# Kernel tuning notes

Measured on AMD Instinct MI355X. Metric: run time of the kernel, lower is better.

The kernel has to match this reference:

```python
import jax, jax.numpy as jnp
import numpy as np

N_NODES = 50000
N_EDGES = 800000
VOCAB = 4096          # node_emb_size
EMB_DIM = 128         # node_emb_dim
HIDDEN = 128          # hidden_dim -> layer1 out = 2*HIDDEN
N_POS = 1024


def gcn_conv(h, edge_index, W, b, n):
    """PyG GCNConv: lin -> add self loops -> sym-normalized scatter-add -> +bias."""
    h = h @ W                                   # [N, out]
    row, col = edge_index[0], edge_index[1]     # source, target
    loop = jnp.arange(n)
    row = jnp.concatenate([row, loop])
    col = jnp.concatenate([col, loop])
    deg = jax.ops.segment_sum(jnp.ones(row.shape[0], dtype=h.dtype), col, num_segments=n)
    dinv = jnp.where(deg > 0, jax.lax.rsqrt(deg), 0.0)
    norm = dinv[row] * dinv[col]                # [E+N]
    msg = h[row] * norm[:, None]                # gather + scale
    return jax.ops.segment_sum(msg, col, num_segments=n) + b


def setup_inputs() -> dict:
    key = jax.random.key(0)
    ks = jax.random.split(key, 10)
    x = jax.random.randint(ks[0], (N_NODES, 1), 0, VOCAB)
    edge_index = jax.random.randint(ks[1], (2, N_EDGES), 0, N_NODES)
    x_position = jax.random.randint(ks[2], (N_POS,), 0, N_NODES)
    # Embedding init: normal(0, emb_dim^-0.5) per initialize_parameters
    emb = jax.random.normal(ks[3], (VOCAB, EMB_DIM), jnp.float32) * EMB_DIM ** -0.5
    # GCN / linear weights (glorot-ish)
    W1 = jax.random.normal(ks[4], (EMB_DIM, 2 * HIDDEN), jnp.float32) * (EMB_DIM ** -0.5)
    b1 = jnp.zeros((2 * HIDDEN,), jnp.float32)
    W2 = jax.random.normal(ks[5], (2 * HIDDEN, HIDDEN), jnp.float32) * ((2 * HIDDEN) ** -0.5)
    b2 = jnp.zeros((HIDDEN,), jnp.float32)
    Wc = jax.random.normal(ks[6], (HIDDEN, VOCAB), jnp.float32) * (HIDDEN ** -0.5)
    bc = jnp.zeros((VOCAB,), jnp.float32)
    return {"x": x, "edge_index": edge_index, "x_position": x_position,
            "emb": emb, "W1": W1, "b1": b1, "W2": W2, "b2": b2, "Wc": Wc, "bc": bc}


def reference(x, edge_index, x_position, emb, W1, b1, W2, b2, Wc, bc):
    n = x.shape[0]
    h = emb[x[:, 0]]                                   # Embedding + squeeze(1)
    h = jax.nn.relu(gcn_conv(h, edge_index, W1, b1, n))
    z = gcn_conv(h, edge_index, W2, b2, n)             # [N, HIDDEN]
    logits = z @ Wc + bc                               # classifier over all nodes
    # embedding stage: mean of classified rows at x_position, keep dim 0
    return jnp.mean(logits[x_position], axis=0, keepdims=True)  # [1, VOCAB]
```

## Files before the change

### kernel.cpp

```cpp
#include <hip/hip_runtime.h>

constexpr int EMB  = 128;
constexpr int H1D  = 256;
constexpr int H2D  = 128;
constexpr int VOC  = 4096;
constexpr int NSL  = 32;
constexpr int RPB  = 16;

__global__ void k_pre(const float* __restrict__ emb, const float* __restrict__ W1,
                      float* __restrict__ embW1,
                      const int* __restrict__ xpos, int* count, unsigned int* flagbits,
                      int* cnt, unsigned int* needw, float* wagg, float* wsum,
                      int* nflag, int* total, int np, int n, int nwords) {
    int t = threadIdx.x;
    int b = blockIdx.x;
    if (b < VOC / RPB) {
        __shared__ float er[RPB][EMB];
        int r0 = b * RPB;
        for (int i = t; i < RPB * EMB; i += 256) {
            er[i / EMB][i % EMB] = emb[(size_t)r0 * EMB + i];
        }
        __syncthreads();
        float acc[RPB];
#pragma unroll
        for (int rr = 0; rr < RPB; rr++) acc[rr] = 0.0f;
        for (int k = 0; k < EMB; k++) {
            float w = W1[k * H1D + t];
#pragma unroll
            for (int rr = 0; rr < RPB; rr++) acc[rr] += er[rr][k] * w;
        }
#pragma unroll
        for (int rr = 0; rr < RPB; rr++) {
            embW1[(size_t)(r0 + rr) * H1D + t] = acc[rr];
        }
        return;
    }
    if (b == VOC / RPB) {
        for (int i = t; i < n; i += 256) count[i] = 0;
        for (int i = t; i < nwords; i += 256) flagbits[i] = 0u;
        __syncthreads();
        for (int p = t; p < np; p += 256) {
            int v = xpos[p];
            atomicAdd(&count[v], 1);
            atomicOr(&flagbits[v >> 5], 1u << (v & 31));
        }
        return;
    }
    int i = (b - (VOC / RPB + 1)) * 256 + t;
    if (i < n) { cnt[i] = 0; wagg[i] = 0.0f; }
    if (i < nwords) needw[i] = 0u;
    if (i < NSL * H1D) wsum[i] = 0.0f;
    if (i == 0) { *nflag = 0; *total = 0; }
}

__global__ void k_hist(const int* __restrict__ row, const int* __restrict__ col,
                       const unsigned int* __restrict__ flagbits, int* cnt,
                       unsigned int* markw, int ne) {
    int e = blockIdx.x * blockDim.x + threadIdx.x;
    int base = e * 4;
    if (base + 3 < ne) {
        int4 c4 = ((const int4*)col)[e];
        atomicAdd(&cnt[c4.x], 1);
        atomicAdd(&cnt[c4.y], 1);
        atomicAdd(&cnt[c4.z], 1);
        atomicAdd(&cnt[c4.w], 1);
        bool f0 = (flagbits[c4.x >> 5] >> (c4.x & 31)) & 1u;
        bool f1 = (flagbits[c4.y >> 5] >> (c4.y & 31)) & 1u;
        bool f2 = (flagbits[c4.z >> 5] >> (c4.z & 31)) & 1u;
        bool f3 = (flagbits[c4.w >> 5] >> (c4.w & 31)) & 1u;
        if (f0 | f1 | f2 | f3) {
            int4 r4 = ((const int4*)row)[e];
            if (f0) atomicOr(&markw[r4.x >> 5], 1u << (r4.x & 31));
            if (f1) atomicOr(&markw[r4.y >> 5], 1u << (r4.y & 31));
            if (f2) atomicOr(&markw[r4.z >> 5], 1u << (r4.z & 31));
            if (f3) atomicOr(&markw[r4.w >> 5], 1u << (r4.w & 31));
        }
    } else {
        for (int q = base; q < ne; q++) {
            int c = col[q];
            atomicAdd(&cnt[c], 1);
            if ((flagbits[c >> 5] >> (c & 31)) & 1u) {
                int r = row[q];
                atomicOr(&markw[r >> 5], 1u << (r & 31));
            }
        }
    }
}

__global__ void k_alloc(unsigned int* needw,
                        const unsigned int* __restrict__ flagbits,
                        const int* __restrict__ cnt, const int* __restrict__ count,
                        const int* __restrict__ x, int2* __restrict__ pk,
                        float* wagg, int* needlist, int* nflag, int* total,
                        int* offs, int* cursor, int n) {
    int v = blockIdx.x * blockDim.x + threadIdx.x;
    int lane = threadIdx.x & 63;
    int cv = 0;
    bool need = false;
    if (v < n) {
        cv = cnt[v];
        float dv = rsqrtf((float)cv + 1.0f);
        int2 p; p.x = x[v]; p.y = __float_as_int(dv);
        pk[v] = p;
        bool mark = (needw[v >> 5] >> (v & 31)) & 1u;
        bool flag = (flagbits[v >> 5] >> (v & 31)) & 1u;
        need = mark || flag;
        if (flag) wagg[v] = (float)count[v] / ((float)cv + 1.0f);
    }
    unsigned long long nm = __ballot(need);
    int wbase = (v & ~63) >> 5;
    if (lane == 0)  needw[wbase]     = (unsigned int)(nm & 0xffffffffu);
    if (lane == 32) needw[wbase + 1] = (unsigned int)(nm >> 32);
    int seg = need ? cv : 0;
    int incl = seg;
#pragma unroll
    for (int d = 1; d < 64; d <<= 1) {
        int t = __shfl_up(incl, d);
        if (lane >= d) incl += t;
    }
    int excl = incl - seg;
    int wave_total = __shfl(incl, 63);
    int rank = __popcll(nm & ((1ull << lane) - 1));
    int wcnt = __popcll(nm);
    int base_id = 0, base_off = 0;
    if (lane == 0) {
        if (wcnt > 0) base_id = atomicAdd(nflag, wcnt);
        if (wave_total > 0) base_off = atomicAdd(total, wave_total);
    }
    base_id  = __shfl(base_id, 0);
    base_off = __shfl(base_off, 0);
    if (need) {
        needlist[base_id + rank] = v;
        int o = base_off + excl;
        offs[v] = o;
        cursor[v] = o;
    }
}

__global__ void k_scatter(const int* __restrict__ row, const int* __restrict__ col,
                          const unsigned int* __restrict__ needw,
                          const unsigned int* __restrict__ flagbits,
                          const int* __restrict__ count,
                          const int2* __restrict__ pk,
                          int* cursor, int2* srowp, float* wagg, int ne) {
    int e = blockIdx.x * blockDim.x + threadIdx.x;
    int base = e * 4;
    auto doedge = [&](int c, int r) {
        if ((needw[c >> 5] >> (c & 31)) & 1u) {
            int pos = atomicAdd(&cursor[c], 1);
            int2 pr = pk[r];
            srowp[pos] = pr;
            if ((flagbits[c >> 5] >> (c & 31)) & 1u) {
                float dc = __int_as_float(pk[c].y);
                atomicAdd(&wagg[r], (float)count[c] * dc * __int_as_float(pr.y));
            }
        }
    };
    if (base + 3 < ne) {
        int4 c4 = ((const int4*)col)[e];
        int4 r4 = ((const int4*)row)[e];
        doedge(c4.x, r4.x);
        doedge(c4.y, r4.y);
        doedge(c4.z, r4.z);
        doedge(c4.w, r4.w);
    } else {
        for (int q = base; q < ne; q++) doedge(col[q], row[q]);
    }
}

__global__ void k_fconv(const int* __restrict__ needlist, const int* __restrict__ nneed_p,
                        const float* __restrict__ wagg, const int2* __restrict__ pk,
                        const int2* __restrict__ srowp,
                        const int* __restrict__ offs, const int* __restrict__ cnt,
                        const float* __restrict__ embW1, const float* __restrict__ b1,
                        float* __restrict__ wsum) {
    int lane = threadIdx.x & 63;
    int wib  = threadIdx.x >> 6;
    int wid  = blockIdx.x * (blockDim.x >> 6) + wib;
    int nw   = gridDim.x * (blockDim.x >> 6);
    int nn   = *nneed_p;
    const float4* __restrict__ ew = (const float4*)embW1;
    float4 bfrag = ((const float4*)b1)[lane];
    float4 acc2 = {0.0f, 0.0f, 0.0f, 0.0f};

    for (int i = wid; i < nn; i += nw) {
        int v = needlist[i];
        int2 pv = pk[v];
        float dv = __int_as_float(pv.y);
        float wa = wagg[v];
        float4 s = ew[(size_t)pv.x * 64 + lane];
        float w0 = dv * dv;
        float4 acc;
        acc.x = bfrag.x + w0 * s.x;
        acc.y = bfrag.y + w0 * s.y;
        acc.z = bfrag.z + w0 * s.z;
        acc.w = bfrag.w + w0 * s.w;
        int start = offs[v], m = cnt[v];
        for (int base = 0; base < m; base += 64) {
            int mm = min(64, m - base);
            int xr = 0; float wr = 0.0f;
            if (lane < mm) {
                int2 pke = srowp[start + base + lane];
                xr = pke.x;
                wr = __int_as_float(pke.y) * dv;
            }
            int e = 0;
            for (; e + 4 <= mm; e += 4) {
                int i0 = __shfl(xr, e),     i1 = __shfl(xr, e + 1);
                int i2 = __shfl(xr, e + 2), i3 = __shfl(xr, e + 3);
                float q0 = __shfl(wr, e),     q1 = __shfl(wr, e + 1);
                float q2 = __shfl(wr, e + 2), q3 = __shfl(wr, e + 3);
                float4 t0 = ew[(size_t)i0 * 64 + lane];
                float4 t1 = ew[(size_t)i1 * 64 + lane];
                float4 t2 = ew[(size_t)i2 * 64 + lane];
                float4 t3 = ew[(size_t)i3 * 64 + lane];
                acc.x += q0 * t0.x + q1 * t1.x + q2 * t2.x + q3 * t3.x;
                acc.y += q0 * t0.y + q1 * t1.y + q2 * t2.y + q3 * t3.y;
                acc.z += q0 * t0.z + q1 * t1.z + q2 * t2.z + q3 * t3.z;
                acc.w += q0 * t0.w + q1 * t1.w + q2 * t2.w + q3 * t3.w;
            }
            for (; e < mm; e++) {
                int i0 = __shfl(xr, e);
                float q0 = __shfl(wr, e);
                float4 t0 = ew[(size_t)i0 * 64 + lane];
                acc.x += q0 * t0.x;
                acc.y += q0 * t0.y;
                acc.z += q0 * t0.z;
                acc.w += q0 * t0.w;
            }
        }
        acc2.x += wa * fmaxf(acc.x, 0.0f);
        acc2.y += wa * fmaxf(acc.y, 0.0f);
        acc2.z += wa * fmaxf(acc.z, 0.0f);
        acc2.w += wa * fmaxf(acc.w, 0.0f);
    }

    __shared__ float red[4][H1D];
    red[wib][4 * lane + 0] = acc2.x;
    red[wib][4 * lane + 1] = acc2.y;
    red[wib][4 * lane + 2] = acc2.z;
    red[wib][4 * lane + 3] = acc2.w;
    __syncthreads();
    int t = threadIdx.x;
    float ssum = red[0][t] + red[1][t] + red[2][t] + red[3][t];
    atomicAdd(&wsum[(blockIdx.x & (NSL - 1)) * H1D + t], ssum);
}

__global__ void k_zout(const float* __restrict__ wsum, const float* __restrict__ W2,
                       const float* __restrict__ b2, const float* __restrict__ Wc,
                       const float* __restrict__ bc, float* __restrict__ out,
                       float inv_np) {
    __shared__ float ws[H1D];
    __shared__ float z[H2D];
    int t = threadIdx.x;
    float s = 0.0f;
#pragma unroll
    for (int c = 0; c < NSL; c++) s += wsum[c * H1D + t];
    ws[t] = s;
    __syncthreads();
    if (t < H2D) {
        float acc = 0.0f;
#pragma unroll 8
        for (int k = 0; k < H1D; k++) acc += ws[k] * W2[k * H2D + t];
        z[t] = b2[t] + acc * inv_np;
    }
    __syncthreads();
    int c = blockIdx.x * blockDim.x + t;
    float acc = bc[c];
#pragma unroll 8
    for (int j = 0; j < H2D; j++) acc += z[j] * Wc[(size_t)j * VOC + c];
    out[c] = acc;
}

extern "C" void kernel_launch(void* const* d_in, const int* in_sizes, int n_in,
                              void* d_out, int out_size, void* d_ws, size_t ws_size,
                              hipStream_t stream) {
    const int n  = in_sizes[0];
    const int ne = in_sizes[1] / 2;
    const int np = in_sizes[2];

    const int*   x    = (const int*)d_in[0];
    const int*   ei   = (const int*)d_in[1];
    const int*   xpos = (const int*)d_in[2];
    const float* emb  = (const float*)d_in[3];
    const float* W1   = (const float*)d_in[4];
    const float* b1   = (const float*)d_in[5];
    const float* W2   = (const float*)d_in[6];
    const float* b2   = (const float*)d_in[7];
    const float* Wc   = (const float*)d_in[8];
    const float* bc   = (const float*)d_in[9];
    float*       out  = (float*)d_out;

    const int* row = ei;
    const int* col = ei + ne;

    char* p = (char*)d_ws;
    auto alloc = [&](size_t bytes) {
        char* r = p;
        p += (bytes + 255) & ~(size_t)255;
        return r;
    };
    const int nb     = (n + 255) / 256;
    const int nwords = nb * 8;

    int*          cnt      = (int*)alloc((size_t)n * 4);
    int*          offs     = (int*)alloc((size_t)n * 4);
    int*          cursor   = (int*)alloc((size_t)n * 4);
    int*          count    = (int*)alloc((size_t)n * 4);
    int*          needlist = (int*)alloc((size_t)n * 4);
    unsigned int* needw    = (unsigned int*)alloc((size_t)nwords * 4);
    unsigned int* flagbits = (unsigned int*)alloc((size_t)nwords * 4);
    int2*         pk       = (int2*)alloc((size_t)n * 8);
    int2*         srowp    = (int2*)alloc((size_t)ne * 8);
    int*          nflag    = (int*)alloc(256 * 4);
    int*          total    = (int*)alloc(256 * 4);
    float*        wagg     = (float*)alloc((size_t)n * 4);
    float*        embW1    = (float*)alloc((size_t)VOC * H1D * 4);
    float*        wsum     = (float*)alloc((size_t)NSL * H1D * 4);

    const int ne4  = (ne + 3) / 4;
    const int neb4 = (ne4 + 255) / 256;

    k_pre<<<VOC / RPB + 1 + nb, 256, 0, stream>>>(emb, W1, embW1, xpos, count, flagbits,
                                                  cnt, needw, wagg, wsum, nflag, total,
                                                  np, n, nwords);
    k_hist<<<neb4, 256, 0, stream>>>(row, col, flagbits, cnt, needw, ne);
    k_alloc<<<nb, 256, 0, stream>>>(needw, flagbits, cnt, count, x, pk, wagg,
                                    needlist, nflag, total, offs, cursor, n);
    k_scatter<<<neb4, 256, 0, stream>>>(row, col, needw, flagbits, count, pk,
                                        cursor, srowp, wagg, ne);
    k_fconv<<<2048, 256, 0, stream>>>(needlist, nflag, wagg, pk, srowp, offs, cnt,
                                      embW1, b1, wsum);
    k_zout<<<VOC / 256, 256, 0, stream>>>(wsum, W2, b2, Wc, bc, out, 1.0f / (float)np);
}
```

Baseline: 192.9 us.

## Fuse all stages into one cooperative persistent kernel with grid syncs

```diff
diff --git a/kernel.cpp b/kernel.cpp
--- a/kernel.cpp
+++ b/kernel.cpp
@@ -1,4 +1,7 @@
 #include <hip/hip_runtime.h>
+#include <hip/hip_cooperative_groups.h>
+
+namespace cg = cooperative_groups;
 
 constexpr int EMB  = 128;
 constexpr int H1D  = 256;
@@ -6,6 +9,301 @@
 constexpr int VOC  = 4096;
 constexpr int NSL  = 32;
 constexpr int RPB  = 16;
+constexpr int NBLK = 512;
+constexpr int NT   = NBLK * 256;
+constexpr int KGS  = 4;
+
+struct MegaP {
+    const float* emb; const float* W1; float* embW1;
+    const int* xpos; int* count; unsigned int* flagbits;
+    int* cnt; unsigned int* needw; float* wagg; float* wsum;
+    int* nflag; int* total;
+    const int* row; const int* col;
+    const int* x; int2* pk;
+    int* needlist; int* offs; int* cursor; int2* srowp;
+    const float* b1; const float* W2; const float* b2;
+    const float* Wc; const float* bc; float* out;
+    float inv_np;
+    int n, ne, np, nwords;
+};
+
+__global__ void __launch_bounds__(256, 2) k_mega(MegaP P) {
+    cg::grid_group grid = cg::this_grid();
+    const int t   = threadIdx.x;
+    const int b   = blockIdx.x;
+    const int tid = b * 256 + t;
+    const int lane = t & 63;
+
+    __shared__ float er[RPB][EMB];
+    __shared__ float red[4][H1D];
+    __shared__ float wsl[H1D];
+    __shared__ float zl[H2D];
+
+    if (b < VOC / RPB) {
+        int r0 = b * RPB;
+        for (int i = t; i < RPB * EMB; i += 256)
+            er[i / EMB][i % EMB] = P.emb[(size_t)r0 * EMB + i];
+        __syncthreads();
+        float acc[RPB];
+#pragma unroll
+        for (int rr = 0; rr < RPB; rr++) acc[rr] = 0.0f;
+        for (int k = 0; k < EMB; k++) {
+            float w = P.W1[k * H1D + t];
+#pragma unroll
+            for (int rr = 0; rr < RPB; rr++) acc[rr] += er[rr][k] * w;
+        }
+#pragma unroll
+        for (int rr = 0; rr < RPB; rr++)
+            P.embW1[(size_t)(r0 + rr) * H1D + t] = acc[rr];
+    } else if (b == NBLK - 1) {
+        for (int i = t; i < P.n; i += 256) P.count[i] = 0;
+        for (int i = t; i < P.nwords; i += 256) P.flagbits[i] = 0u;
+        __syncthreads();
+        for (int p = t; p < P.np; p += 256) {
+            int v = P.xpos[p];
+            atomicAdd(&P.count[v], 1);
+            atomicOr(&P.flagbits[v >> 5], 1u << (v & 31));
+        }
+    } else {
+        for (int i = (b - VOC / RPB) * 256 + t; i < P.n; i += (NBLK - 1 - VOC / RPB) * 256) {
+            P.cnt[i] = 0; P.wagg[i] = 0.0f;
+        }
+        int i0 = (b - VOC / RPB) * 256 + t;
+        if (i0 < P.nwords) P.needw[i0] = 0u;
+        if (i0 < NSL * H1D) P.wsum[i0] = 0.0f;
+        if (i0 == 0) { *P.nflag = 0; *P.total = 0; }
+    }
+    grid.sync();
+
+    const int ne4 = P.ne >> 2;
+    int4 c4s[KGS], r4s[KGS];
+#pragma unroll
+    for (int s = 0; s < KGS; s++) {
+        int g = tid + s * NT;
+        if (g < ne4) {
+            c4s[s] = ((const int4*)P.col)[g];
+            r4s[s] = ((const int4*)P.row)[g];
+        }
+    }
+#pragma unroll
+    for (int s = 0; s < KGS; s++) {
+        int g = tid + s * NT;
+        if (g < ne4) {
+            int4 c4 = c4s[s];
+            atomicAdd(&P.cnt[c4.x], 1);
+            atomicAdd(&P.cnt[c4.y], 1);
+            atomicAdd(&P.cnt[c4.z], 1);
+            atomicAdd(&P.cnt[c4.w], 1);
+            bool f0 = (P.flagbits[c4.x >> 5] >> (c4.x & 31)) & 1u;
+            bool f1 = (P.flagbits[c4.y >> 5] >> (c4.y & 31)) & 1u;
+            bool f2 = (P.flagbits[c4.z >> 5] >> (c4.z & 31)) & 1u;
+            bool f3 = (P.flagbits[c4.w >> 5] >> (c4.w & 31)) & 1u;
+            if (f0 | f1 | f2 | f3) {
+                int4 r4 = r4s[s];
+                if (f0) atomicOr(&P.needw[r4.x >> 5], 1u << (r4.x & 31));
+                if (f1) atomicOr(&P.needw[r4.y >> 5], 1u << (r4.y & 31));
+                if (f2) atomicOr(&P.needw[r4.z >> 5], 1u << (r4.z & 31));
+                if (f3) atomicOr(&P.needw[r4.w >> 5], 1u << (r4.w & 31));
+            }
+        }
+    }
+    for (int g = tid + KGS * NT; g < ne4; g += NT) {
+        int4 c4 = ((const int4*)P.col)[g];
+        atomicAdd(&P.cnt[c4.x], 1); atomicAdd(&P.cnt[c4.y], 1);
+        atomicAdd(&P.cnt[c4.z], 1); atomicAdd(&P.cnt[c4.w], 1);
+        int4 r4 = ((const int4*)P.row)[g];
+        if ((P.flagbits[c4.x >> 5] >> (c4.x & 31)) & 1u) atomicOr(&P.needw[r4.x >> 5], 1u << (r4.x & 31));
+        if ((P.flagbits[c4.y >> 5] >> (c4.y & 31)) & 1u) atomicOr(&P.needw[r4.y >> 5], 1u << (r4.y & 31));
+        if ((P.flagbits[c4.z >> 5] >> (c4.z & 31)) & 1u) atomicOr(&P.needw[r4.z >> 5], 1u << (r4.z & 31));
+        if ((P.flagbits[c4.w >> 5] >> (c4.w & 31)) & 1u) atomicOr(&P.needw[r4.w >> 5], 1u << (r4.w & 31));
+    }
+    {
+        int base = ne4 * 4;
+        if (tid < P.ne - base) {
+            int q = base + tid;
+            int c = P.col[q];
+            atomicAdd(&P.cnt[c], 1);
+            if ((P.flagbits[c >> 5] >> (c & 31)) & 1u) {
+                int r = P.row[q];
+                atomicOr(&P.needw[r >> 5], 1u << (r & 31));
+            }
+        }
+    }
+    grid.sync();
+
+    {
+        int iters = (P.n + NT - 1) / NT;
+        for (int it = 0; it < iters; it++) {
+            int v = tid + it * NT;
+            int cv = 0;
+            bool need = false;
+            if (v < P.n) {
+                cv = P.cnt[v];
+                float dv = rsqrtf((float)cv + 1.0f);
+                int2 pp; pp.x = P.x[v]; pp.y = __float_as_int(dv);
+                P.pk[v] = pp;
+                bool mark = (P.needw[v >> 5] >> (v & 31)) & 1u;
+                bool flag = (P.flagbits[v >> 5] >> (v & 31)) & 1u;
+                need = mark || flag;
+                if (flag) P.wagg[v] = (float)P.count[v] / ((float)cv + 1.0f);
+            }
+            unsigned long long nm = __ballot(need);
+            int wbase = (v & ~63) >> 5;
+            if (lane == 0  && wbase < P.nwords)     P.needw[wbase]     = (unsigned int)(nm & 0xffffffffu);
+            if (lane == 32 && wbase + 1 < P.nwords) P.needw[wbase + 1] = (unsigned int)(nm >> 32);
+            int seg = need ? cv : 0;
+            int incl = seg;
+#pragma unroll
+            for (int d = 1; d < 64; d <<= 1) {
+                int u = __shfl_up(incl, d);
+                if (lane >= d) incl += u;
+            }
+            int excl = incl - seg;
+            int wave_total = __shfl(incl, 63);
+            int rank = __popcll(nm & ((1ull << lane) - 1));
+            int wcnt = __popcll(nm);
+            int base_id = 0, base_off = 0;
+            if (lane == 0) {
+                if (wcnt > 0) base_id = atomicAdd(P.nflag, wcnt);
+                if (wave_total > 0) base_off = atomicAdd(P.total, wave_total);
+            }
+            base_id  = __shfl(base_id, 0);
+            base_off = __shfl(base_off, 0);
+            if (need) {
+                P.needlist[base_id + rank] = v;
+                int o = base_off + excl;
+                P.offs[v] = o;
+                P.cursor[v] = o;
+            }
+        }
+    }
+    grid.sync();
+
+    {
+        auto doedge = [&](int c, int r) {
+            if ((P.needw[c >> 5] >> (c & 31)) & 1u) {
+                int pos = atomicAdd(&P.cursor[c], 1);
+                int2 pr = P.pk[r];
+                P.srowp[pos] = pr;
+                if ((P.flagbits[c >> 5] >> (c & 31)) & 1u) {
+                    float dc = __int_as_float(P.pk[c].y);
+                    atomicAdd(&P.wagg[r], (float)P.count[c] * dc * __int_as_float(pr.y));
+                }
+            }
+        };
+#pragma unroll
+        for (int s = 0; s < KGS; s++) {
+            int g = tid + s * NT;
+            if (g < ne4) {
+                doedge(c4s[s].x, r4s[s].x);
+                doedge(c4s[s].y, r4s[s].y);
+                doedge(c4s[s].z, r4s[s].z);
+                doedge(c4s[s].w, r4s[s].w);
+            }
+        }
+        for (int g = tid + KGS * NT; g < ne4; g += NT) {
+            int4 c4 = ((const int4*)P.col)[g];
+            int4 r4 = ((const int4*)P.row)[g];
+            doedge(c4.x, r4.x); doedge(c4.y, r4.y);
+            doedge(c4.z, r4.z); doedge(c4.w, r4.w);
+        }
+        int base = ne4 * 4;
+        if (tid < P.ne - base) {
+            int q = base + tid;
+            doedge(P.col[q], P.row[q]);
+        }
+    }
+    grid.sync();
+
+    {
+        int wib = t >> 6;
+        int wid = b * 4 + wib;
+        int nw  = NBLK * 4;
+        int nn  = *P.nflag;
+        const float4* __restrict__ ew = (const float4*)P.embW1;
+        float4 bfrag = ((const float4*)P.b1)[lane];
+        float4 acc2 = {0.0f, 0.0f, 0.0f, 0.0f};
+        for (int i = wid; i < nn; i += nw) {
+            int v = P.needlist[i];
+            int2 pv = P.pk[v];
+            float dv = __int_as_float(pv.y);
+            float wa = P.wagg[v];
+            float4 s = ew[(size_t)pv.x * 64 + lane];
+            float w0 = dv * dv;
+            float4 acc;
+            acc.x = bfrag.x + w0 * s.x;
+            acc.y = bfrag.y + w0 * s.y;
+            acc.z = bfrag.z + w0 * s.z;
+            acc.w = bfrag.w + w0 * s.w;
+            int start = P.offs[v], m = P.cnt[v];
+            for (int base = 0; base < m; base += 64) {
+                int mm = min(64, m - base);
+                int xr = 0; float wr = 0.0f;
+                if (lane < mm) {
+                    int2 pke = P.srowp[start + base + lane];
+                    xr = pke.x;
+                    wr = __int_as_float(pke.y) * dv;
+                }
+                int e = 0;
+                for (; e + 4 <= mm; e += 4) {
+                    int i0 = __shfl(xr, e),     i1 = __shfl(xr, e + 1);
+                    int i2 = __shfl(xr, e + 2), i3 = __shfl(xr, e + 3);
+                    float q0 = __shfl(wr, e),     q1 = __shfl(wr, e + 1);
+                    float q2 = __shfl(wr, e + 2), q3 = __shfl(wr, e + 3);
+                    float4 t0 = ew[(size_t)i0 * 64 + lane];
+                    float4 t1 = ew[(size_t)i1 * 64 + lane];
+                    float4 t2 = ew[(size_t)i2 * 64 + lane];
+                    float4 t3 = ew[(size_t)i3 * 64 + lane];
+                    acc.x += q0 * t0.x + q1 * t1.x + q2 * t2.x + q3 * t3.x;
+                    acc.y += q0 * t0.y + q1 * t1.y + q2 * t2.y + q3 * t3.y;
+                    acc.z += q0 * t0.z + q1 * t1.z + q2 * t2.z + q3 * t3.z;
+                    acc.w += q0 * t0.w + q1 * t1.w + q2 * t2.w + q3 * t3.w;
+                }
+                for (; e < mm; e++) {
+                    int i0 = __shfl(xr, e);
+                    float q0 = __shfl(wr, e);
+                    float4 t0 = ew[(size_t)i0 * 64 + lane];
+                    acc.x += q0 * t0.x;
+                    acc.y += q0 * t0.y;
+                    acc.z += q0 * t0.z;
+                    acc.w += q0 * t0.w;
+                }
+            }
+            acc2.x += wa * fmaxf(acc.x, 0.0f);
+            acc2.y += wa * fmaxf(acc.y, 0.0f);
+            acc2.z += wa * fmaxf(acc.z, 0.0f);
+            acc2.w += wa * fmaxf(acc.w, 0.0f);
+        }
+        red[wib][4 * lane + 0] = acc2.x;
+        red[wib][4 * lane + 1] = acc2.y;
+        red[wib][4 * lane + 2] = acc2.z;
+        red[wib][4 * lane + 3] = acc2.w;
+        __syncthreads();
+        float ssum = red[0][t] + red[1][t] + red[2][t] + red[3][t];
+        atomicAdd(&P.wsum[(b & (NSL - 1)) * H1D + t], ssum);
+    }
+    grid.sync();
+
+    if (b < VOC / 256) {
+        float s = 0.0f;
+#pragma unroll
+        for (int c = 0; c < NSL; c++) s += P.wsum[c * H1D + t];
+        wsl[t] = s;
+        __syncthreads();
+        if (t < H2D) {
+            float acc = 0.0f;
+#pragma unroll 8
+            for (int k = 0; k < H1D; k++) acc += wsl[k] * P.W2[k * H2D + t];
+            zl[t] = P.b2[t] + acc * P.inv_np;
+        }
+        __syncthreads();
+        int c = b * 256 + t;
+        float acc = P.bc[c];
+#pragma unroll 8
+        for (int j = 0; j < H2D; j++) acc += zl[j] * P.Wc[(size_t)j * VOC + c];
+        P.out[c] = acc;
+    }
+}
 
 __global__ void k_pre(const float* __restrict__ emb, const float* __restrict__ W1,
                       float* __restrict__ embW1,
@@ -17,9 +315,8 @@
     if (b < VOC / RPB) {
         __shared__ float er[RPB][EMB];
         int r0 = b * RPB;
-        for (int i = t; i < RPB * EMB; i += 256) {
+        for (int i = t; i < RPB * EMB; i += 256)
             er[i / EMB][i % EMB] = emb[(size_t)r0 * EMB + i];
-        }
         __syncthreads();
         float acc[RPB];
 #pragma unroll
@@ -30,9 +327,8 @@
             for (int rr = 0; rr < RPB; rr++) acc[rr] += er[rr][k] * w;
         }
 #pragma unroll
-        for (int rr = 0; rr < RPB; rr++) {
+        for (int rr = 0; rr < RPB; rr++)
             embW1[(size_t)(r0 + rr) * H1D + t] = acc[rr];
-        }
         return;
     }
     if (b == VOC / RPB) {
@@ -115,8 +411,8 @@
     int incl = seg;
 #pragma unroll
     for (int d = 1; d < 64; d <<= 1) {
-        int t = __shfl_up(incl, d);
-        if (lane >= d) incl += t;
+        int u = __shfl_up(incl, d);
+        if (lane >= d) incl += u;
     }
     int excl = incl - seg;
     int wave_total = __shfl(incl, 63);
@@ -182,7 +478,6 @@
     const float4* __restrict__ ew = (const float4*)embW1;
     float4 bfrag = ((const float4*)b1)[lane];
     float4 acc2 = {0.0f, 0.0f, 0.0f, 0.0f};
-
     for (int i = wid; i < nn; i += nw) {
         int v = needlist[i];
         int2 pv = pk[v];
@@ -234,7 +529,6 @@
         acc2.z += wa * fmaxf(acc.z, 0.0f);
         acc2.w += wa * fmaxf(acc.w, 0.0f);
     }
-
     __shared__ float red[4][H1D];
     red[wib][4 * lane + 0] = acc2.x;
     red[wib][4 * lane + 1] = acc2.y;
@@ -318,18 +612,34 @@
     float*        embW1    = (float*)alloc((size_t)VOC * H1D * 4);
     float*        wsum     = (float*)alloc((size_t)NSL * H1D * 4);
 
-    const int ne4  = (ne + 3) / 4;
-    const int neb4 = (ne4 + 255) / 256;
-
-    k_pre<<<VOC / RPB + 1 + nb, 256, 0, stream>>>(emb, W1, embW1, xpos, count, flagbits,
-                                                  cnt, needw, wagg, wsum, nflag, total,
-                                                  np, n, nwords);
-    k_hist<<<neb4, 256, 0, stream>>>(row, col, flagbits, cnt, needw, ne);
-    k_alloc<<<nb, 256, 0, stream>>>(needw, flagbits, cnt, count, x, pk, wagg,
-                                    needlist, nflag, total, offs, cursor, n);
-    k_scatter<<<neb4, 256, 0, stream>>>(row, col, needw, flagbits, count, pk,
-                                        cursor, srowp, wagg, ne);
-    k_fconv<<<2048, 256, 0, stream>>>(needlist, nflag, wagg, pk, srowp, offs, cnt,
-                                      embW1, b1, wsum);
-    k_zout<<<VOC / 256, 256, 0, stream>>>(wsum, W2, b2, Wc, bc, out, 1.0f / (float)np);
-}
+    MegaP hp;
+    hp.emb = emb; hp.W1 = W1; hp.embW1 = embW1;
+    hp.xpos = xpos; hp.count = count; hp.flagbits = flagbits;
+    hp.cnt = cnt; hp.needw = needw; hp.wagg = wagg; hp.wsum = wsum;
+    hp.nflag = nflag; hp.total = total;
+    hp.row = row; hp.col = col;
+    hp.x = x; hp.pk = pk;
+    hp.needlist = needlist; hp.offs = offs; hp.cursor = cursor; hp.srowp = srowp;
+    hp.b1 = b1; hp.W2 = W2; hp.b2 = b2; hp.Wc = Wc; hp.bc = bc; hp.out = out;
+    hp.inv_np = 1.0f / (float)np;
+    hp.n = n; hp.ne = ne; hp.np = np; hp.nwords = nwords;
+
+    void* args[] = { &hp };
+    hipError_t err = hipLaunchCooperativeKernel((void*)k_mega, dim3(NBLK), dim3(256),
+                                                args, 0, stream);
+    if (err != hipSuccess) {
+        const int ne4  = (ne + 3) / 4;
+        const int neb4 = (ne4 + 255) / 256;
+        k_pre<<<VOC / RPB + 1 + nb, 256, 0, stream>>>(emb, W1, embW1, xpos, count, flagbits,
+                                                      cnt, needw, wagg, wsum, nflag, total,
+                                                      np, n, nwords);
+        k_hist<<<neb4, 256, 0, stream>>>(row, col, flagbits, cnt, needw, ne);
+        k_alloc<<<nb, 256, 0, stream>>>(needw, flagbits, cnt, count, x, pk, wagg,
+                                        needlist, nflag, total, offs, cursor, n);
+        k_scatter<<<neb4, 256, 0, stream>>>(row, col, needw, flagbits, count, pk,
+                                            cursor, srowp, wagg, ne);
+        k_fconv<<<2048, 256, 0, stream>>>(needlist, nflag, wagg, pk, srowp, offs, cnt,
+                                          embW1, b1, wsum);
+        k_zout<<<VOC / 256, 256, 0, stream>>>(wsum, W2, b2, Wc, bc, out, 1.0f / (float)np);
+    }
+}
```

Result: slower. 483.8 us (+150.8%).
